# Optimization experiments

Hardware: AMD Instinct MI355X
Metric: run time of the kernel (lower is better)

The kernel has to match this reference:

```python
import jax, jax.numpy as jnp
import numpy as np

N_HEADS = 16
ROPE_BASE = 10000.0


def _apply_rope(t, cos, sin):
    # t: (B, H, S, D); cos/sin: (S, D/2). Rotate-half convention.
    d2 = t.shape[-1] // 2
    t1, t2 = t[..., :d2], t[..., d2:]
    return jnp.concatenate([t1 * cos - t2 * sin, t2 * cos + t1 * sin], axis=-1)


def setup_inputs() -> dict:
    key = jax.random.key(0)
    k0, k1, k2, k3, k4 = jax.random.split(key, 5)
    B, S, E = 4, 2048, 1024
    scale = 0.02
    x = jax.random.normal(k0, (B, S, E), dtype=jnp.float32)
    w_qkv = jax.random.normal(k1, (E, 3 * E), dtype=jnp.float32) * scale
    b_qkv = jnp.zeros((3 * E,), dtype=jnp.float32)
    w_proj = jax.random.normal(k2, (E, E), dtype=jnp.float32) * scale
    b_proj = jnp.zeros((E,), dtype=jnp.float32)
    return {"x": x, "w_qkv": w_qkv, "b_qkv": b_qkv, "w_proj": w_proj, "b_proj": b_proj}


def reference(x, w_qkv, b_qkv, w_proj, b_proj):
    B, S, E = x.shape
    H = N_HEADS
    D = E // H
    # fused QKV projection
    qkv = x @ w_qkv + b_qkv                      # (B, S, 3E)
    q, k, v = jnp.split(qkv, 3, axis=-1)
    def to_heads(t):
        return t.reshape(B, S, H, D).transpose(0, 2, 1, 3)  # (B, H, S, D)
    q, k, v = to_heads(q), to_heads(k), to_heads(v)
    # RoPE (rotate-half)
    inv_freq = ROPE_BASE ** (-jnp.arange(0, D, 2, dtype=jnp.float32) / D)  # (D/2,)
    pos = jnp.arange(S, dtype=jnp.float32)
    freqs = pos[:, None] * inv_freq[None, :]     # (S, D/2)
    cos, sin = jnp.cos(freqs), jnp.sin(freqs)
    q = _apply_rope(q, cos, sin)
    k = _apply_rope(k, cos, sin)
    # causal SDPA
    scores = jnp.einsum('bhqd,bhkd->bhqk', q, k) / jnp.sqrt(jnp.float32(D))
    causal = jnp.tril(jnp.ones((S, S), dtype=bool))
    scores = jnp.where(causal, scores, jnp.float32(-1e30))
    probs = jax.nn.softmax(scores, axis=-1)
    out = jnp.einsum('bhqk,bhkd->bhqd', probs, v)  # (B, H, S, D)
    out = out.transpose(0, 2, 1, 3).reshape(B, S, E)
    # output projection (dropout is identity at p=0 / eval)
    return out @ w_proj + b_proj
```

## Files before the change

### kernel.cpp

```cpp
#include <hip/hip_runtime.h>

typedef unsigned short u16;
typedef __bf16 bf16x8 __attribute__((ext_vector_type(8)));
typedef float f32x4 __attribute__((ext_vector_type(4)));

__device__ __forceinline__ u16 f2b(float f) {
    unsigned u = __builtin_bit_cast(unsigned, f);
    unsigned r = (u + 0x7fffu + ((u >> 16) & 1u)) >> 16;
    return (u16)r;
}
#if __has_builtin(__builtin_amdgcn_cvt_pk_bf16_f32)
typedef __bf16 bf16x2_t __attribute__((ext_vector_type(2)));
__device__ __forceinline__ unsigned pk2(float a, float b) {
    return __builtin_bit_cast(unsigned, __builtin_amdgcn_cvt_pk_bf16_f32(a, b));
}
#else
__device__ __forceinline__ unsigned pk2(float a, float b) {
    return (unsigned)f2b(a) | ((unsigned)f2b(b) << 16);
}
#endif
#if __has_builtin(__builtin_amdgcn_exp2f)
#define EXP2F(x) __builtin_amdgcn_exp2f(x)
#else
#define EXP2F(x) exp2f(x)
#endif

__device__ __forceinline__ void gl_lds16(const u16* g, u16* l) {
    __builtin_amdgcn_global_load_lds(
        (const __attribute__((address_space(1))) unsigned*)(const void*)g,
        (__attribute__((address_space(3))) unsigned*)(void*)l, 16, 0, 0);
}

__global__ __launch_bounds__(256) void k_convert(const float* __restrict__ in,
                                                 u16* __restrict__ out, int n8) {
    int i = blockIdx.x * 256 + threadIdx.x;
    if (i >= n8) return;
    const float4* p = (const float4*)(in + (size_t)i * 8);
    float4 a = p[0], b = p[1];
    u16 t[8] = {f2b(a.x), f2b(a.y), f2b(a.z), f2b(a.w),
                f2b(b.x), f2b(b.y), f2b(b.z), f2b(b.w)};
    *(uint4*)(out + (size_t)i * 8) = *(const uint4*)t;
}

__global__ __launch_bounds__(256) void k_transpose_bf16(const float* __restrict__ in,
                                                        u16* __restrict__ out,
                                                        int R, int C) {
    __shared__ u16 tile[64][72];
    int tc = blockIdx.x * 64;
    int tr = blockIdx.y * 64;
    for (int i = threadIdx.x; i < 4096; i += 256) {
        int r = i >> 6, c = i & 63;
        tile[c][r] = f2b(in[(size_t)(tr + r) * C + tc + c]);
    }
    __syncthreads();
    for (int i = threadIdx.x; i < 4096; i += 256) {
        int r = i >> 6, c = i & 63;
        out[(size_t)(tc + r) * R + tr + c] = tile[r][c];
    }
}

__device__ __forceinline__ void gemm_mainloop(const u16* __restrict__ Ab,
                                              const u16* __restrict__ Bb, int K,
                                              u16* As, u16* Bs, int tid,
                                              f32x4 (&acc)[4][4]) {
    const int wave = tid >> 6, lane = tid & 63;
    const int col = lane & 15, quad = lane >> 4;
    const int wm = wave >> 1, wn = wave & 1;
    const int lrow = lane >> 2, lk = (lane & 3) * 8;
    u16* ldsA0 = As + (wave * 16) * 32;
    u16* ldsA1 = As + (64 + wave * 16) * 32;
    u16* ldsB0 = Bs + (wave * 16) * 32;
    u16* ldsB1 = Bs + (64 + wave * 16) * 32;
    const u16* gA0 = Ab + (size_t)(wave * 16 + lrow) * K + lk;
    const u16* gA1 = gA0 + (size_t)64 * K;
    const u16* gB0 = Bb + (size_t)(wave * 16 + lrow) * K + lk;
    const u16* gB1 = gB0 + (size_t)64 * K;
    for (int k0 = 0; k0 < K; k0 += 64) {
        if (k0) __syncthreads();
#pragma unroll
        for (int kh = 0; kh < 2; ++kh) {
            int ko = k0 + kh * 32;
            gl_lds16(gA0 + ko, ldsA0 + kh * 4096);
            gl_lds16(gA1 + ko, ldsA1 + kh * 4096);
            gl_lds16(gB0 + ko, ldsB0 + kh * 4096);
            gl_lds16(gB1 + ko, ldsB1 + kh * 4096);
        }
        __syncthreads();
#pragma unroll
        for (int kh = 0; kh < 2; ++kh) {
            bf16x8 af[4], bfr[4];
#pragma unroll
            for (int mt = 0; mt < 4; ++mt)
                af[mt] = *(const bf16x8*)(As + kh * 4096 +
                                          (wm * 64 + mt * 16 + col) * 32 + quad * 8);
#pragma unroll
            for (int nt = 0; nt < 4; ++nt)
                bfr[nt] = *(const bf16x8*)(Bs + kh * 4096 +
                                           (wn * 64 + nt * 16 + col) * 32 + quad * 8);
#pragma unroll
            for (int mt = 0; mt < 4; ++mt)
#pragma unroll
                for (int nt = 0; nt < 4; ++nt)
                    acc[mt][nt] = __builtin_amdgcn_mfma_f32_16x16x32_bf16(
                        af[mt], bfr[nt], acc[mt][nt], 0, 0, 0);
        }
    }
}

__global__ __launch_bounds__(256) void k_gemm_qkv_rope(
    const u16* __restrict__ A, const u16* __restrict__ Bt,
    const float* __restrict__ bias, u16* __restrict__ Qr, u16* __restrict__ Kr,
    u16* __restrict__ Vt) {
    __shared__ __align__(16) u16 As[2 * 128 * 32];
    __shared__ __align__(16) u16 Bs[2 * 128 * 32];
    const int K = 1024;
    int tid = threadIdx.x;
    int lane = tid & 63, wave = tid >> 6;
    int col = lane & 15, quad = lane >> 4;
    int wm = wave >> 1, wn = wave & 1;
    int mBase = blockIdx.y * 128;
    int nBase = blockIdx.x * 128;
    f32x4 acc[4][4] = {};
    gemm_mainloop(A + (size_t)mBase * K, Bt + (size_t)nBase * K, K, As, Bs, tid, acc);

    int n64 = nBase + wn * 64;
    int region = n64 >> 10;
    int h = (n64 & 1023) >> 6;
    if (region < 2) {
        u16* out = (region == 0) ? Qr : Kr;
        float qs = (region == 0) ? 0.18033688011112042f : 1.0f;
        const float C0 = 0.4152410118609203f;
#pragma unroll
        for (int nt = 0; nt < 2; ++nt) {
            int d1 = nt * 16 + col;
            float inv_freq = exp2f(-C0 * (float)d1);
            float b1 = bias[n64 + nt * 16 + col];
            float b2 = bias[n64 + nt * 16 + col + 32];
#pragma unroll
            for (int mt = 0; mt < 4; ++mt) {
                int mrow = mBase + wm * 64 + mt * 16 + quad * 4;
#pragma unroll
                for (int r = 0; r < 4; ++r) {
                    int m = mrow + r;
                    int s = m & 2047, b = m >> 11;
                    float sn, cs;
                    sincosf((float)s * inv_freq, &sn, &cs);
                    float t1 = acc[mt][nt][r] + b1;
                    float t2 = acc[mt][nt + 2][r] + b2;
                    size_t base = ((size_t)((b * 16 + h) * 2048 + s)) * 64;
                    out[base + d1] = f2b((t1 * cs - t2 * sn) * qs);
                    out[base + d1 + 32] = f2b((t2 * cs + t1 * sn) * qs);
                }
            }
        }
    } else {
#pragma unroll
        for (int nt = 0; nt < 4; ++nt) {
            int d = nt * 16 + col;
            float bv = bias[n64 + nt * 16 + col];
#pragma unroll
            for (int mt = 0; mt < 4; ++mt) {
                int mrow = mBase + wm * 64 + mt * 16 + quad * 4;
#pragma unroll
                for (int r = 0; r < 4; ++r) {
                    int m = mrow + r;
                    int s = m & 2047, b = m >> 11;
                    Vt[((size_t)((b * 16 + h) * 64 + d)) * 2048 + s] =
                        f2b(acc[mt][nt][r] + bv);
                }
            }
        }
    }
}

__global__ __launch_bounds__(256) void k_attn(const u16* __restrict__ Qr,
                                              const u16* __restrict__ Kr,
                                              const u16* __restrict__ Vt,
                                              u16* __restrict__ O) {
    __shared__ __align__(16) u16 Ks[64 * 72];
    __shared__ __align__(16) u16 Vs[64 * 72];
    int tid = threadIdx.x, wave = tid >> 6, lane = tid & 63;
    int col = lane & 15, quad = lane >> 4;
    int bx = blockIdx.x, bh = blockIdx.y;
    int b = bh >> 4, h = bh & 15;
    size_t headQ = (size_t)bh * 2048 * 64;
    size_t headV = (size_t)bh * 64 * 2048;
    int r0 = tid >> 3, kc = tid & 7;
    int rb72 = ((col >> 2) * 8 + (col & 3)) * 72;

    for (int half = 0; half < 2; ++half) {
        int qb = half ? bx : (15 - bx);
        int t0 = 2 * qb, t1 = t0 + 1;
        int myq0 = qb * 128 + wave * 16 + col;
        int myq1 = myq0 + 64;
        const u16* qp0 = Qr + headQ + (size_t)myq0 * 64;
        const u16* qp1 = Qr + headQ + (size_t)myq1 * 64;
        bf16x8 aq00 = *(const bf16x8*)(qp0 + quad * 8);
        bf16x8 aq01 = *(const bf16x8*)(qp0 + 32 + quad * 8);
        bf16x8 aq10 = *(const bf16x8*)(qp1 + quad * 8);
        bf16x8 aq11 = *(const bf16x8*)(qp1 + 32 + quad * 8);
        f32x4 o0[4] = {}, o1[4] = {};
        float l0 = 0.f, l1 = 0.f;

        for (int j = 0; j <= t1; ++j) {
            bool d0 = (j <= t0);
            __syncthreads();
            {
                const u16* kg = Kr + headQ + (size_t)(j * 64 + r0) * 64 + kc * 8;
                const u16* vg = Vt + headV + (size_t)r0 * 2048 + j * 64 + kc * 8;
                *(uint4*)(Ks + r0 * 72 + kc * 8) = *(const uint4*)kg;
                *(uint4*)(Ks + (r0 + 32) * 72 + kc * 8) = *(const uint4*)(kg + 32 * 64);
                *(uint4*)(Vs + r0 * 72 + kc * 8) = *(const uint4*)vg;
                *(uint4*)(Vs + (r0 + 32) * 72 + kc * 8) = *(const uint4*)(vg + 32 * 2048);
            }
            __syncthreads();
            f32x4 s0[4], s1[4];
#pragma unroll
            for (int nt = 0; nt < 4; ++nt) {
                const u16* kp = Ks + rb72 + ((nt & 1) * 32 + (nt >> 1) * 4) * 72;
                bf16x8 ak0 = *(const bf16x8*)(kp + quad * 8);
                bf16x8 ak1 = *(const bf16x8*)(kp + 32 + quad * 8);
                if (d0) {
                    f32x4 z = {};
                    z = __builtin_amdgcn_mfma_f32_16x16x32_bf16(ak0, aq00, z, 0, 0, 0);
                    s0[nt] = __builtin_amdgcn_mfma_f32_16x16x32_bf16(ak1, aq01, z, 0, 0, 0);
                }
                f32x4 z = {};
                z = __builtin_amdgcn_mfma_f32_16x16x32_bf16(ak0, aq10, z, 0, 0, 0);
                s1[nt] = __builtin_amdgcn_mfma_f32_16x16x32_bf16(ak1, aq11, z, 0, 0, 0);
            }
            if (j == t0) {
#pragma unroll
                for (int nt = 0; nt < 4; ++nt) {
                    int keyb = j * 64 + (nt & 1) * 32 + quad * 8 + (nt >> 1) * 4;
#pragma unroll
                    for (int r = 0; r < 4; ++r)
                        if (keyb + r > myq0) s0[nt][r] = -3.0e38f;
                }
            }
            if (j == t1) {
#pragma unroll
                for (int nt = 0; nt < 4; ++nt) {
                    int keyb = j * 64 + (nt & 1) * 32 + quad * 8 + (nt >> 1) * 4;
#pragma unroll
                    for (int r = 0; r < 4; ++r)
                        if (keyb + r > myq1) s1[nt][r] = -3.0e38f;
                }
            }
            unsigned P40[8], P41[8];
            if (d0) {
#pragma unroll
                for (int nt = 0; nt < 4; ++nt) {
                    float p0 = EXP2F(s0[nt][0]);
                    float p1 = EXP2F(s0[nt][1]);
                    float p2 = EXP2F(s0[nt][2]);
                    float p3 = EXP2F(s0[nt][3]);
                    l0 += (p0 + p1) + (p2 + p3);
                    P40[2 * nt] = pk2(p0, p1);
                    P40[2 * nt + 1] = pk2(p2, p3);
                }
            }
#pragma unroll
            for (int nt = 0; nt < 4; ++nt) {
                float p0 = EXP2F(s1[nt][0]);
                float p1 = EXP2F(s1[nt][1]);
                float p2 = EXP2F(s1[nt][2]);
                float p3 = EXP2F(s1[nt][3]);
                l1 += (p0 + p1) + (p2 + p3);
                P41[2 * nt] = pk2(p0, p1);
                P41[2 * nt + 1] = pk2(p2, p3);
            }
#pragma unroll
            for (int kk = 0; kk < 2; ++kk) {
                uint4 bw0, bw1;
                bw0.x = P40[2 * kk];
                bw0.y = P40[2 * kk + 1];
                bw0.z = P40[2 * kk + 4];
                bw0.w = P40[2 * kk + 5];
                bw1.x = P41[2 * kk];
                bw1.y = P41[2 * kk + 1];
                bw1.z = P41[2 * kk + 4];
                bw1.w = P41[2 * kk + 5];
                bf16x8 bp0 = __builtin_bit_cast(bf16x8, bw0);
                bf16x8 bp1 = __builtin_bit_cast(bf16x8, bw1);
#pragma unroll
                for (int mt = 0; mt < 4; ++mt) {
                    bf16x8 av = *(const bf16x8*)(Vs + (mt * 16 + col) * 72 + kk * 32 + quad * 8);
                    if (d0)
                        o0[mt] = __builtin_amdgcn_mfma_f32_16x16x32_bf16(av, bp0, o0[mt], 0, 0, 0);
                    o1[mt] = __builtin_amdgcn_mfma_f32_16x16x32_bf16(av, bp1, o1[mt], 0, 0, 0);
                }
            }
        }
        l0 += __shfl_xor(l0, 16);
        l0 += __shfl_xor(l0, 32);
        l1 += __shfl_xor(l1, 16);
        l1 += __shfl_xor(l1, 32);
        float inv0 = 1.0f / l0, inv1 = 1.0f / l1;
        u16* orow0 = O + (size_t)(b * 2048 + myq0) * 1024 + h * 64;
        u16* orow1 = O + (size_t)(b * 2048 + myq1) * 1024 + h * 64;
#pragma unroll
        for (int mt = 0; mt < 4; ++mt) {
            uint2 w0, w1;
            w0.x = pk2(o0[mt][0] * inv0, o0[mt][1] * inv0);
            w0.y = pk2(o0[mt][2] * inv0, o0[mt][3] * inv0);
            w1.x = pk2(o1[mt][0] * inv1, o1[mt][1] * inv1);
            w1.y = pk2(o1[mt][2] * inv1, o1[mt][3] * inv1);
            *(uint2*)(orow0 + mt * 16 + quad * 4) = w0;
            *(uint2*)(orow1 + mt * 16 + quad * 4) = w1;
        }
    }
}

__global__ __launch_bounds__(256) void k_gemm_proj(const u16* __restrict__ A,
                                                   const u16* __restrict__ Bt,
                                                   const float* __restrict__ bias,
                                                   float* __restrict__ out) {
    __shared__ __align__(16) u16 As[2 * 128 * 32];
    __shared__ __align__(16) u16 Bs[2 * 128 * 32];
    const int K = 1024;
    int tid = threadIdx.x;
    int lane = tid & 63, wave = tid >> 6;
    int col = lane & 15, quad = lane >> 4;
    int wm = wave >> 1, wn = wave & 1;
    int mBase = blockIdx.y * 128;
    int nBase = blockIdx.x * 128;
    f32x4 acc[4][4] = {};
    gemm_mainloop(A + (size_t)mBase * K, Bt + (size_t)nBase * K, K, As, Bs, tid, acc);
#pragma unroll
    for (int nt = 0; nt < 4; ++nt) {
        int n = nBase + wn * 64 + nt * 16 + col;
        float bv = bias[n];
#pragma unroll
        for (int mt = 0; mt < 4; ++mt) {
            int m = mBase + wm * 64 + mt * 16 + quad * 4;
#pragma unroll
            for (int r = 0; r < 4; ++r)
                out[(size_t)(m + r) * 1024 + n] = acc[mt][nt][r] + bv;
        }
    }
}

extern "C" void kernel_launch(void* const* d_in, const int* in_sizes, int n_in,
                              void* d_out, int out_size, void* d_ws, size_t ws_size,
                              hipStream_t stream) {
    const float* x = (const float*)d_in[0];
    const float* w_qkv = (const float*)d_in[1];
    const float* b_qkv = (const float*)d_in[2];
    const float* w_proj = (const float*)d_in[3];
    const float* b_proj = (const float*)d_in[4];
    float* out = (float*)d_out;
    char* ws = (char*)d_ws;
    u16* x_bf = (u16*)(ws);
    u16* wqkvT = (u16*)(ws + 16777216);
    u16* wprojT = (u16*)(ws + 23068672);
    u16* Qr = (u16*)(ws + 25165824);
    u16* Kr = (u16*)(ws + 41943040);
    u16* Vt = (u16*)(ws + 58720256);
    u16* AO = (u16*)(ws + 75497472);

    k_convert<<<4096, 256, 0, stream>>>(x, x_bf, 1048576);
    k_transpose_bf16<<<dim3(48, 16), 256, 0, stream>>>(w_qkv, wqkvT, 1024, 3072);
    k_transpose_bf16<<<dim3(16, 16), 256, 0, stream>>>(w_proj, wprojT, 1024, 1024);
    k_gemm_qkv_rope<<<dim3(24, 64), 256, 0, stream>>>(x_bf, wqkvT, b_qkv, Qr, Kr, Vt);
    k_attn<<<dim3(8, 64), 256, 0, stream>>>(Qr, Kr, Vt, AO);
    k_gemm_proj<<<dim3(8, 64), 256, 0, stream>>>(AO, wprojT, b_proj, out);
}
```

Baseline: 278.8 us.

## Precompute RoPE table, stage Q/K epilogue through LDS, vectorize V stores

A new small kernel precomputes a cos/sin table for every (position, frequency) pair. The QKV GEMM epilogue reads this table instead of calling sincosf per element. Q/K results are now written into swizzled shared memory, then stored to global memory as coalesced 16-byte rows instead of scattered 2-byte stores. V-transpose stores pack four bf16 values into 8-byte writes. This adds one extra launch and two block barriers, and the table sits in the attention-output buffer region, which is safe only because that buffer is written later.

Result: no change. 276.1 us (-1.0%).

```diff
diff --git a/kernel.cpp b/kernel.cpp
--- a/kernel.cpp
+++ b/kernel.cpp
@@ -29,6 +29,16 @@
     __builtin_amdgcn_global_load_lds(
         (const __attribute__((address_space(1))) unsigned*)(const void*)g,
         (__attribute__((address_space(3))) unsigned*)(void*)l, 16, 0, 0);
+}
+
+__global__ __launch_bounds__(256) void k_rope_table(float2* __restrict__ tab) {
+    int i = blockIdx.x * 256 + threadIdx.x;
+    int s = i >> 5, d = i & 31;
+    const float C0 = 0.4152410118609203f;
+    float inv_freq = exp2f(-C0 * (float)d);
+    float sn, cs;
+    sincosf((float)s * inv_freq, &sn, &cs);
+    tab[i] = make_float2(cs, sn);
 }
 
 __global__ __launch_bounds__(256) void k_convert(const float* __restrict__ in,
@@ -109,10 +119,11 @@
 
 __global__ __launch_bounds__(256) void k_gemm_qkv_rope(
     const u16* __restrict__ A, const u16* __restrict__ Bt,
-    const float* __restrict__ bias, u16* __restrict__ Qr, u16* __restrict__ Kr,
-    u16* __restrict__ Vt) {
-    __shared__ __align__(16) u16 As[2 * 128 * 32];
-    __shared__ __align__(16) u16 Bs[2 * 128 * 32];
+    const float* __restrict__ bias, const float2* __restrict__ tab,
+    u16* __restrict__ Qr, u16* __restrict__ Kr, u16* __restrict__ Vt) {
+    __shared__ __align__(16) u16 smem[16384];
+    u16* As = smem;
+    u16* Bs = smem + 8192;
     const int K = 1024;
     int tid = threadIdx.x;
     int lane = tid & 63, wave = tid >> 6;
@@ -123,51 +134,65 @@
     f32x4 acc[4][4] = {};
     gemm_mainloop(A + (size_t)mBase * K, Bt + (size_t)nBase * K, K, As, Bs, tid, acc);
 
+    int region = nBase >> 10;
     int n64 = nBase + wn * 64;
-    int region = n64 >> 10;
     int h = (n64 & 1023) >> 6;
     if (region < 2) {
-        u16* out = (region == 0) ? Qr : Kr;
+        __syncthreads();
         float qs = (region == 0) ? 0.18033688011112042f : 1.0f;
-        const float C0 = 0.4152410118609203f;
 #pragma unroll
         for (int nt = 0; nt < 2; ++nt) {
             int d1 = nt * 16 + col;
-            float inv_freq = exp2f(-C0 * (float)d1);
-            float b1 = bias[n64 + nt * 16 + col];
-            float b2 = bias[n64 + nt * 16 + col + 32];
+            float b1 = bias[n64 + d1];
+            float b2 = bias[n64 + d1 + 32];
+            int nl = wn * 64 + nt * 16 + col;
 #pragma unroll
             for (int mt = 0; mt < 4; ++mt) {
-                int mrow = mBase + wm * 64 + mt * 16 + quad * 4;
+                int mlb = wm * 64 + mt * 16 + quad * 4;
 #pragma unroll
                 for (int r = 0; r < 4; ++r) {
-                    int m = mrow + r;
-                    int s = m & 2047, b = m >> 11;
-                    float sn, cs;
-                    sincosf((float)s * inv_freq, &sn, &cs);
+                    int mloc = mlb + r;
+                    int s = (mBase + mloc) & 2047;
+                    float2 t = tab[s * 32 + d1];
                     float t1 = acc[mt][nt][r] + b1;
                     float t2 = acc[mt][nt + 2][r] + b2;
-                    size_t base = ((size_t)((b * 16 + h) * 2048 + s)) * 64;
-                    out[base + d1] = f2b((t1 * cs - t2 * sn) * qs);
-                    out[base + d1 + 32] = f2b((t2 * cs + t1 * sn) * qs);
-                }
-            }
+                    int sw = (mloc & 7) << 3;
+                    smem[mloc * 128 + (nl ^ sw)] = f2b((t1 * t.x - t2 * t.y) * qs);
+                    smem[mloc * 128 + ((nl + 32) ^ sw)] = f2b((t2 * t.x + t1 * t.y) * qs);
+                }
+            }
+        }
+        __syncthreads();
+        u16* outp = (region == 0) ? Qr : Kr;
+#pragma unroll
+        for (int p = 0; p < 8; ++p) {
+            int lin = p * 256 + tid;
+            int mloc = lin >> 4;
+            int c8 = (lin & 15) << 3;
+            uint4 v = *(const uint4*)(smem + mloc * 128 + (c8 ^ ((mloc & 7) << 3)));
+            int m = mBase + mloc;
+            int s = m & 2047, b = m >> 11;
+            int ng = (nBase & 1023) + c8;
+            *(uint4*)(Qr == outp || Kr == outp
+                          ? outp + ((size_t)((b * 16 + (ng >> 6)) * 2048 + s)) * 64 +
+                                (ng & 63)
+                          : outp) = v;
         }
     } else {
+        int b = mBase >> 11;
+        int sb0 = mBase & 2047;
 #pragma unroll
         for (int nt = 0; nt < 4; ++nt) {
             int d = nt * 16 + col;
-            float bv = bias[n64 + nt * 16 + col];
+            float bv = bias[n64 + d];
+            u16* vrow = Vt + ((size_t)((b * 16 + h) * 64 + d)) * 2048;
 #pragma unroll
             for (int mt = 0; mt < 4; ++mt) {
-                int mrow = mBase + wm * 64 + mt * 16 + quad * 4;
-#pragma unroll
-                for (int r = 0; r < 4; ++r) {
-                    int m = mrow + r;
-                    int s = m & 2047, b = m >> 11;
-                    Vt[((size_t)((b * 16 + h) * 64 + d)) * 2048 + s] =
-                        f2b(acc[mt][nt][r] + bv);
-                }
+                int s = sb0 + wm * 64 + mt * 16 + quad * 4;
+                uint2 w;
+                w.x = pk2(acc[mt][nt][0] + bv, acc[mt][nt][1] + bv);
+                w.y = pk2(acc[mt][nt][2] + bv, acc[mt][nt][3] + bv);
+                *(uint2*)(vrow + s) = w;
             }
         }
     }
@@ -358,11 +383,13 @@
     u16* Kr = (u16*)(ws + 41943040);
     u16* Vt = (u16*)(ws + 58720256);
     u16* AO = (u16*)(ws + 75497472);
-
+    float2* tab = (float2*)(ws + 75497472);
+
+    k_rope_table<<<256, 256, 0, stream>>>(tab);
     k_convert<<<4096, 256, 0, stream>>>(x, x_bf, 1048576);
     k_transpose_bf16<<<dim3(48, 16), 256, 0, stream>>>(w_qkv, wqkvT, 1024, 3072);
     k_transpose_bf16<<<dim3(16, 16), 256, 0, stream>>>(w_proj, wprojT, 1024, 1024);
-    k_gemm_qkv_rope<<<dim3(24, 64), 256, 0, stream>>>(x_bf, wqkvT, b_qkv, Qr, Kr, Vt);
+    k_gemm_qkv_rope<<<dim3(24, 64), 256, 0, stream>>>(x_bf, wqkvT, b_qkv, tab, Qr, Kr, Vt);
     k_attn<<<dim3(8, 64), 256, 0, stream>>>(Qr, Kr, Vt, AO);
     k_gemm_proj<<<dim3(8, 64), 256, 0, stream>>>(AO, wprojT, b_proj, out);
 }
```
